# Performance work log

Measured on AMD Instinct MI355X. Metric: run time of the kernel, lower is better.

Reference implementation:

```python
import jax, jax.numpy as jnp
import numpy as np
from jax import lax

EPOCHS = 3
D_IN, D_OUT = 20, 18
_BN_EPS = 1e-5
_RECT_EPS = 1e-4


def _sym(a):
    return 0.5 * (a + jnp.swapaxes(a, -1, -2))


def _logm(a):
    s, u = jnp.linalg.eigh(_sym(a))
    return jnp.einsum('...ij,...j,...kj->...ik', u, jnp.log(s), u)


def _expm(a):
    s, u = jnp.linalg.eigh(_sym(a))
    return jnp.einsum('...ij,...j,...kj->...ik', u, jnp.exp(s), u)


def _rectify(a):
    # SPDRectified: clamp eigenvalues at epsilon
    s, u = jnp.linalg.eigh(_sym(a))
    s = jnp.maximum(s, _RECT_EPS)
    return jnp.einsum('...ij,...j,...kj->...ik', u, s, u)


def _bn(x, g, b):
    # training-mode BatchNorm2d (biased variance, as torch uses for normalization)
    m = x.mean(axis=(0, 2, 3), keepdims=True)
    v = x.var(axis=(0, 2, 3), keepdims=True)
    return (x - m) * lax.rsqrt(v + _BN_EPS) * g[None, :, None, None] + b[None, :, None, None]


def _patch_lens(n, epochs):
    base = n // epochs
    lens = [base] * epochs
    for i in range(n - base * epochs):
        lens[i] += 1
    return lens


def _forward(x, conv1_w, conv1_b, bn1_g, bn1_b, conv2_w, conv2_b, bn2_g, bn2_b,
             Wq, Wk, Wv, lin_w, lin_b):
    B = x.shape[0]
    # conv1: Conv2d(1, 22, (22, 1)) -- full contraction over the 22 EEG channels
    h = jnp.einsum('oh,bht->bot', conv1_w, x[:, 0]) + conv1_b[None, :, None]
    h = _bn(h[:, :, None, :], bn1_g, bn1_b)  # (B,22,1,T)
    # conv2: Conv2d(22, 20, (1, 12), padding=(0, 6)) -> time length T+1
    h = lax.conv_general_dilated(h, conv2_w, (1, 1), [(0, 0), (6, 6)],
                                 dimension_numbers=('NCHW', 'OIHW', 'NCHW'))
    h = h + conv2_b[None, :, None, None]
    h = _bn(h, bn2_g, bn2_b)
    sig = h[:, :, 0, :]  # (B, 20, T+1)
    # E2R: split time axis into EPOCHS patches, trace-normalized covariance per patch
    covs, off = [], 0
    eye = jnp.eye(D_IN, dtype=x.dtype)
    for L in _patch_lens(sig.shape[-1], EPOCHS):
        seg = sig[:, :, off:off + L]
        off += L
        seg = seg - seg.mean(axis=-1, keepdims=True)
        c = seg @ jnp.swapaxes(seg, -1, -2) / (L - 1)
        c = c / jnp.trace(c, axis1=-2, axis2=-1)[:, None, None]
        covs.append(c + 1e-5 * eye)
    cov = jnp.stack(covs, axis=1)  # (B, EPOCHS, 20, 20)
    # SPDTransform (bilinear congruence W^T X W) for Q, K, V
    Q = jnp.einsum('ia,bmij,jc->bmac', Wq, cov, Wq)
    K = jnp.einsum('ia,bmij,jc->bmac', Wk, cov, Wk)
    V = jnp.einsum('ia,bmij,jc->bmac', Wv, cov, Wv)
    logQ, logK, logV = _logm(Q), _logm(K), _logm(V)
    # log-Euclidean distance: sum of singular values of D D^T == ||D||_F^2
    # energy[b, i, j] = || logK[b,i] - logQ[b,j] ||_F^2 (matches the repeat/expand layout)
    diff = logK[:, :, None] - logQ[:, None, :]  # (B, m, m, d, d)
    energy = jnp.sum(diff * diff, axis=(-1, -2))  # (B, m, m)
    f = 1.0 / (1.0 + jnp.log1p(energy))
    prob = jax.nn.softmax(f, axis=-2)      # softmax over dim=-2 (the K index)
    prob = jnp.swapaxes(prob, -1, -2)      # permute(0, 2, 1)
    # LogEuclideanMean: weighted mean in log domain, then matrix exp
    mean_log = jnp.einsum('bpi,bikl->bpkl', prob, logV)
    out = _expm(mean_log)
    out = _rectify(out)
    tang = _logm(out)
    ri, ci = np.triu_indices(D_OUT)
    feat = tang[:, :, ri, ci].reshape(B, -1)  # (B, EPOCHS * 171)
    return feat @ lin_w.T + lin_b


def setup_inputs():
    key = jax.random.key(0)
    ks = jax.random.split(key, 16)
    B, C, T = 1024, 22, 438
    f32 = jnp.float32
    return {
        'x': jax.random.normal(ks[0], (B, 1, C, T), f32),
        'conv1_w': 0.1 * jax.random.normal(ks[1], (22, 22), f32),
        'conv1_b': 0.1 * jax.random.normal(ks[2], (22,), f32),
        'bn1_g': 1.0 + 0.1 * jax.random.normal(ks[3], (22,), f32),
        'bn1_b': 0.1 * jax.random.normal(ks[4], (22,), f32),
        'conv2_w': 0.05 * jax.random.normal(ks[5], (20, 22, 1, 12), f32),
        'conv2_b': 0.1 * jax.random.normal(ks[6], (20,), f32),
        'bn2_g': 1.0 + 0.1 * jax.random.normal(ks[7], (20,), f32),
        'bn2_b': 0.1 * jax.random.normal(ks[8], (20,), f32),
        'Wq': jnp.linalg.qr(jax.random.normal(ks[9], (20, 18), f32))[0],
        'Wk': jnp.linalg.qr(jax.random.normal(ks[10], (20, 18), f32))[0],
        'Wv': jnp.linalg.qr(jax.random.normal(ks[11], (20, 18), f32))[0],
        'lin_w': 0.05 * jax.random.normal(ks[12], (4, 9 * 19 * EPOCHS), f32),
        'lin_b': jnp.zeros((4,), f32),
    }


def reference(x, conv1_w, conv1_b, bn1_g, bn1_b, conv2_w, conv2_b, bn2_g, bn2_b,
              Wq, Wk, Wv, lin_w, lin_b):
    return _forward(x, conv1_w, conv1_b, bn1_g, bn1_b, conv2_w, conv2_b,
                    bn2_g, bn2_b, Wq, Wk, Wv, lin_w, lin_b)
```

## Files before the change

kernel.cpp:

```cpp
#include <hip/hip_runtime.h>
#include <cmath>

#define B_ 1024
#define CIN_ 22
#define T1_ 438
#define COUT_ 20
#define T2_ 439

#define OFF_S 0
#define OFF_M 32
#define OFF_SUM2 576
#define OFF_SSQ2 608
#define OFF_A2 640
#define OFF_ACC_END 704
#define OFF_C 1024
#define OFF_WEFF (OFF_C + B_*3*400)
#define OFF_BPRE (OFF_WEFF + 5280)

__global__ __launch_bounds__(256) void k_zero(float* ws){
  for(int i=threadIdx.x; i<OFF_ACC_END; i+=256) ws[i]=0.f;
}

__global__ __launch_bounds__(256) void k_moment(const float* __restrict__ x, float* __restrict__ ws){
  __shared__ float xs[CIN_][440];
  int b=blockIdx.x;
  const float* xb = x + (size_t)b*CIN_*T1_;
  for(int i=threadIdx.x;i<CIN_*T1_;i+=256){
    int h=i/T1_, t=i-h*T1_;
    xs[h][t]=xb[i];
  }
  if(threadIdx.x<CIN_){ xs[threadIdx.x][438]=0.f; xs[threadIdx.x][439]=0.f; }
  __syncthreads();
  for(int tgt=threadIdx.x; tgt<275; tgt+=256){
    if(tgt<253){
      int r=tgt, i=0;
      while(true){ int c=CIN_-i; if(r<c) break; r-=c; i++; }
      int j=i+r;
      const float4* ri=(const float4*)&xs[i][0];
      const float4* rj=(const float4*)&xs[j][0];
      float acc=0.f;
      for(int t=0;t<110;t++){
        float4 a=ri[t], bb=rj[t];
        acc += a.x*bb.x + a.y*bb.y + a.z*bb.z + a.w*bb.w;
      }
      atomicAdd(&ws[OFF_M + i*CIN_ + j], acc);
    } else {
      int c=tgt-253;
      const float4* rc=(const float4*)&xs[c][0];
      float acc=0.f;
      for(int t=0;t<110;t++){
        float4 a=rc[t];
        acc += a.x + a.y + a.z + a.w;
      }
      atomicAdd(&ws[OFF_S + c], acc);
    }
  }
}

__global__ __launch_bounds__(256) void k_prep(const float* __restrict__ w1, const float* __restrict__ cb1,
                                              const float* __restrict__ g1, const float* __restrict__ bb1,
                                              const float* __restrict__ w2, float* __restrict__ ws){
  __shared__ float a1s[CIN_], e1s[CIN_];
  int tid=threadIdx.x;
  if(tid<CIN_){
    int c=tid;
    const double N = (double)B_*T1_;
    double wS=0.0, wMw=0.0;
    for(int h=0;h<CIN_;h++) wS += (double)w1[c*CIN_+h]*(double)ws[OFF_S+h];
    for(int h=0;h<CIN_;h++){
      for(int h2=0;h2<CIN_;h2++){
        int i=h<h2?h:h2, j=h<h2?h2:h;
        wMw += (double)w1[c*CIN_+h]*(double)w1[c*CIN_+h2]*(double)ws[OFF_M+i*CIN_+j];
      }
    }
    double bc=cb1[c];
    double mean=wS/N+bc;
    double ex2=(wMw+2.0*bc*wS)/N+bc*bc;
    double var=ex2-mean*mean;
    double a1=(double)g1[c]/sqrt(var+1e-5);
    double d1=(double)bb1[c]-mean*a1;
    a1s[c]=(float)a1;
    e1s[c]=(float)(a1*bc+d1);
  }
  __syncthreads();
  for(int idx=tid; idx<5280; idx+=256){
    int o=idx/264, r=idx-o*264, h=r/12, k=r-h*12;
    float s=0.f;
    for(int i=0;i<CIN_;i++) s += w2[(o*CIN_+i)*12+k]*a1s[i]*w1[i*CIN_+h];
    ws[OFF_WEFF+idx]=s;
  }
  if(tid<COUT_){
    float pre=0.f;
    ws[OFF_BPRE+tid*13+0]=0.f;
    for(int k=0;k<12;k++){
      float wb=0.f;
      for(int i=0;i<CIN_;i++) wb += w2[(tid*CIN_+i)*12+k]*e1s[i];
      pre += wb;
      ws[OFF_BPRE+tid*13+k+1]=pre;
    }
  }
}

__global__ __launch_bounds__(256) void k_cov(const float* __restrict__ x,
                                             float* __restrict__ ws){
  __shared__ float Wl[5280];
  __shared__ float preL[COUT_][13];
  __shared__ float xs[CIN_][168];
  __shared__ float h2w[COUT_][156];
  __shared__ float pmu[COUT_];
  int b=blockIdx.x, tid=threadIdx.x;
  for(int i=tid;i<5280;i+=256) Wl[i]=ws[OFF_WEFF+i];
  for(int i=tid;i<260;i+=256) ((float*)preL)[i]=ws[OFF_BPRE+i];
  int pi=0,pj=0;
  if(tid<210){ int r=tid,i=0; while(true){int c=COUT_-i; if(r<c)break; r-=c; i++;} pi=i; pj=i+r; }
  int sc = tid-210;
  float ac1=0.f, ac2=0.f;
  const float* xb = x + (size_t)b*CIN_*T1_;
  int o = tid/12, cch = tid-12*o;
  int t0 = cch*13;
  for(int p=0;p<3;p++){
    const int off = (p==0)?0:((p==1)?147:293);
    const int L = (p==0)?147:146;
    __syncthreads();
    for(int idx=tid; idx<CIN_*168; idx+=256){
      int h=idx/168, c2=idx-h*168;
      int gxt = off-6+c2;
      xs[h][c2] = (c2<167 && gxt>=0 && gxt<T1_) ? xb[h*T1_+gxt] : 0.f;
    }
    __syncthreads();
    if(tid<240){
      float acc[13];
      #pragma unroll
      for(int j=0;j<13;j++){
        int gt = off+t0+j;
        int kmin = 6-gt; kmin = kmin<0?0:kmin;
        int kmax = 443-gt; kmax = kmax>11?11:kmax;
        acc[j] = (kmax>=kmin)? preL[o][kmax+1]-preL[o][kmin] : 0.f;
      }
      const float* Wo = &Wl[o*264];
      for(int h=0;h<CIN_;h++){
        float xw[24];
        #pragma unroll
        for(int c2=0;c2<24;c2++) xw[c2]=xs[h][t0+c2];
        const float* Wh = Wo + h*12;
        #pragma unroll
        for(int k=0;k<12;k++){
          float w=Wh[k];
          #pragma unroll
          for(int j=0;j<13;j++) acc[j] += w*xw[j+k];
        }
      }
      #pragma unroll
      for(int j=0;j<13;j++) if(t0+j<L) h2w[o][t0+j]=acc[j];
    } else {
      int npad = 156-L;
      for(int z=tid-240; z<COUT_*npad; z+=16){
        int oo=z/npad, c2=z-oo*npad;
        h2w[oo][L+c2]=0.f;
      }
    }
    __syncthreads();
    float s=0.f;
    if(tid<210){
      const float4* ri=(const float4*)&h2w[pi][0];
      const float4* rj=(const float4*)&h2w[pj][0];
      for(int t=0;t<39;t++){
        float4 a=ri[t], bb=rj[t];
        s += a.x*bb.x + a.y*bb.y + a.z*bb.z + a.w*bb.w;
      }
    } else if(sc>=0 && sc<COUT_){
      const float4* rc=(const float4*)&h2w[sc][0];
      float s1=0.f,s2=0.f;
      for(int t=0;t<39;t++){
        float4 a=rc[t];
        s1 += a.x+a.y+a.z+a.w;
        s2 += a.x*a.x+a.y*a.y+a.z*a.z+a.w*a.w;
      }
      ac1+=s1; ac2+=s2; pmu[sc]=s1/(float)L;
    }
    __syncthreads();
    if(tid<210){
      s -= (float)L*pmu[pi]*pmu[pj];
      float* Cb = ws + OFF_C + ((size_t)b*3+p)*400;
      Cb[pi*COUT_+pj]=s; Cb[pj*COUT_+pi]=s;
    }
  }
  if(sc>=0 && sc<COUT_){
    atomicAdd(&ws[OFF_SUM2+sc], ac1);
    atomicAdd(&ws[OFF_SSQ2+sc], ac2);
  }
}

__global__ void k_fin2(const float* __restrict__ g2, float* __restrict__ ws){
  int c=threadIdx.x; if(c>=COUT_) return;
  const double N=(double)B_*T2_;
  double m=ws[OFF_SUM2+c]/N;
  double v=ws[OFF_SSQ2+c]/N - m*m;
  ws[OFF_A2+c]=(float)((double)g2[c]/sqrt(v+1e-5));
}

__device__ __forceinline__ void bl_jacobi18(float own[18], float &dgo,
                                            int l18, int gb, bool act, int maxsweep){
  int self = gb + l18;
  for(int sweep=0; sweep<maxsweep; sweep++){
    { float d0=0.f,d1=0.f;
      #pragma unroll
      for(int k=0;k<18;k+=2){ d0+=own[k]*own[k]; d1+=own[k+1]*own[k+1]; }
      dgo=d0+d1;
    }
    float smax=0.f;
    for(int r=0;r<17;r++){
      int t = 2*r - l18;
      t += (t<0)?17:0;
      t -= (t>=17)?17:0;
      int pa = (l18==17)? r : ((t==l18)?17:t);
      int src = act ? (gb + pa) : self;
      float oth[18];
      #pragma unroll
      for(int k=0;k<18;k++) oth[k]=__shfl(own[k], src);
      float dgx = __shfl(dgo, src);
      float a0=0.f,a1=0.f;
      #pragma unroll
      for(int k=0;k<18;k+=2){ a0+=own[k]*oth[k]; a1+=own[k+1]*oth[k+1]; }
      float apq=a0+a1;
      bool isP = l18 < pa;
      float dgp = isP? dgo : dgx;
      float dgq = isP? dgx : dgo;
      float tau = __fdividef(dgq-dgp, 2.f*apq);
      float tt  = __fdividef(copysignf(1.f,tau), fabsf(tau)+sqrtf(1.f+tau*tau));
      float c   = rsqrtf(1.f+tt*tt);
      float s   = tt*c;
      bool  z   = (apq==0.f) || !act;
      tt=z?0.f:tt; c=z?1.f:c; s=z?0.f:s;
      smax=fmaxf(smax,fabsf(s));
      float sgn = isP ? -s : s;
      #pragma unroll
      for(int k=0;k<18;k++) own[k] = c*own[k] + sgn*oth[k];
      dgo = isP ? (dgp - tt*apq) : (dgq + tt*apq);
    }
    if(__all(smax<3e-3f)) break;
  }
  float d0=0.f,d1=0.f;
  #pragma unroll
  for(int k=0;k<18;k+=2){ d0+=own[k]*own[k]; d1+=own[k+1]*own[k+1]; }
  dgo=d0+d1;
}

#define F_A2S 0
#define F_WA 20
#define F_CS 1100
#define F_TT 2300
#define F_TRS 3434
#define F_LTR 3437
#define F_LG 3440
#define F_E9 6356
#define F_PROB 6365
#define F_SC 20
#define F_GL1 3098
#define F_ML 20
#define F_MC2 992
#define F_GL2 2018
#define F_FEAT 3440

__global__ __launch_bounds__(192) void k_fused(const float* __restrict__ Wq,
                                               const float* __restrict__ Wk,
                                               const float* __restrict__ Wv,
                                               const float* __restrict__ lw,
                                               const float* __restrict__ lb,
                                               float* __restrict__ ws,
                                               float* __restrict__ out){
  __shared__ float S[6374];
  int b=blockIdx.x, tid=threadIdx.x;
  int w=tid>>6, wl=tid&63;
  if(tid<20) S[F_A2S+tid]=ws[OFF_A2+tid];
  __syncthreads();
  for(int i=tid;i<1080;i+=192){
    int m=i/360, r=i-m*360, row=r/18;
    const float* W=(m==0)?Wq:((m==1)?Wk:Wv);
    S[F_WA+i]=W[r]*S[F_A2S+row];
  }
  {
    const float* Cb=ws+OFF_C+((size_t)b*3+w)*400;
    for(int i=wl;i<400;i+=64) S[F_CS+w*400+i]=Cb[i];
  }
  if(wl==0){
    float tr=0.f;
    #pragma unroll
    for(int i=0;i<20;i++) tr += S[F_CS+w*400+i*20+i]*S[F_A2S+i]*S[F_A2S+i];
    S[F_TRS+w]=tr;
    S[F_LTR+w]=logf(tr);
  }
  __syncthreads();
  for(int m=0;m<3;m++){
    const float* Wm=S+F_WA+m*360;
    const float* Cw=S+F_CS+w*400;
    float* Tw=S+F_TT+w*378;
    for(int idx=wl; idx<360; idx+=64){
      int a=idx/20, j=idx-a*20;
      float s=0.f;
      for(int i=0;i<20;i++) s += Wm[i*18+a]*Cw[i*20+j];
      Tw[a*21+j]=s;
    }
    __syncthreads();
    for(int idx=wl; idx<324; idx+=64){
      int a=idx/18, c=idx-a*18;
      float s=0.f;
      for(int j=0;j<20;j++) s += Tw[a*21+j]*Wm[j*18+c];
      S[F_LG + m*972 + w*324 + idx]=s;
    }
    __syncthreads();
  }
  int g=wl/18, l18=wl-18*g;
  bool act=(g<3);
  float tr_w=S[F_TRS+w], ltr_w=S[F_LTR+w];
  float sh=1e-5f*tr_w;
  float own[18], dgo=0.f;
  if(act){
    const float* Ag=S+F_LG+g*972+w*324;
    #pragma unroll
    for(int k=0;k<18;k++)
      own[k]=0.5f*(Ag[k*18+l18]+Ag[l18*18+k]) + ((k==l18)?sh:0.f);
  } else {
    #pragma unroll
    for(int k=0;k<18;k++) own[k]=0.f;
  }
  __syncthreads();
  bl_jacobi18(own,dgo,l18,g*18,act,8);
  float dp=fmaxf(dgo,1e-30f);
  float gv=__fdividef(0.5f*logf(dp)-ltr_w, dp);
  float* Mc1=S+F_SC+w*1026;
  float* gl1=S+F_GL1+w*54;
  if(act){
    #pragma unroll
    for(int k=0;k<18;k++) Mc1[g*342 + k*19 + l18]=own[k];
    gl1[g*18+l18]=gv;
  }
  if(wl<54){
    int mat=g, i=l18;
    float w18[18];
    #pragma unroll
    for(int k=0;k<18;k++) w18[k]=gl1[mat*18+k]*Mc1[mat*342+i*19+k];
    float* ob=S+F_LG+mat*972+w*324+i*18;
    for(int j=0;j<18;j++){
      float s=0.f;
      #pragma unroll
      for(int k=0;k<18;k++) s += w18[k]*Mc1[mat*342+j*19+k];
      ob[j]=s;
    }
  }
  __syncthreads();
  if(tid<36){
    int d=tid>>2, sub=tid&3;
    int ii=d/3, p=d-ii*3;
    const float* kk=S+F_LG+972+ii*324+sub*81;
    const float* qq=S+F_LG+p*324+sub*81;
    float s=0.f;
    for(int el=0;el<81;el++){ float dd=kk[el]-qq[el]; s+=dd*dd; }
    s += __shfl_xor(s,1); s += __shfl_xor(s,2);
    if(sub==0) S[F_E9+d]=s;
  }
  __syncthreads();
  if(tid<3){
    int p=tid;
    float f0=1.f/(1.f+log1pf(S[F_E9+0+p]));
    float f1=1.f/(1.f+log1pf(S[F_E9+3+p]));
    float f2=1.f/(1.f+log1pf(S[F_E9+6+p]));
    float mx=fmaxf(f0,fmaxf(f1,f2));
    float x0=expf(f0-mx), x1=expf(f1-mx), x2=expf(f2-mx);
    float inv=1.f/(x0+x1+x2);
    S[F_PROB+p*3+0]=x0*inv; S[F_PROB+p*3+1]=x1*inv; S[F_PROB+p*3+2]=x2*inv;
  }
  __syncthreads();
  for(int idx=tid; idx<972; idx+=192){
    int p=idx/324, el=idx-p*324;
    const float* LV=S+F_LG+1944;
    S[F_ML+idx]=S[F_PROB+p*3+0]*LV[el]+S[F_PROB+p*3+1]*LV[324+el]+S[F_PROB+p*3+2]*LV[648+el];
  }
  __syncthreads();
  bool act2=(wl<18);
  float own2[18], dgo2=0.f;
  if(act2){
    const float* Ag=S+F_ML+w*324;
    #pragma unroll
    for(int k=0;k<18;k++)
      own2[k]=0.5f*(Ag[k*18+wl]+Ag[wl*18+k]) + ((k==wl)?12.f:0.f);
  } else {
    #pragma unroll
    for(int k=0;k<18;k++) own2[k]=0.f;
  }
  bl_jacobi18(own2,dgo2,wl,0,act2,8);
  float lam=sqrtf(fmaxf(dgo2,1e-12f));
  float gv2=__fdividef(fmaxf(lam-12.f,-9.2103404f), fmaxf(dgo2,1e-12f));
  if(act2){
    #pragma unroll
    for(int k=0;k<18;k++) S[F_MC2 + w*342 + k*19 + wl]=own2[k];
    S[F_GL2 + w*18 + wl]=gv2;
  }
  __syncthreads();
  if(tid<54){
    int mat=tid/18, i=tid-mat*18;
    float w18[18];
    #pragma unroll
    for(int k=0;k<18;k++) w18[k]=S[F_GL2+mat*18+k]*S[F_MC2+mat*342+i*19+k];
    int base = mat*171 + (i*18 - (i*(i-1))/2) - i;
    for(int j=i;j<18;j++){
      float s=0.f;
      #pragma unroll
      for(int k=0;k<18;k++) s += w18[k]*S[F_MC2+mat*342+j*19+k];
      S[F_FEAT+base+j]=s;
    }
  }
  __syncthreads();
  if(tid<64){
    int j4 = tid&3, chunk = tid>>2;
    float s=0.f;
    const float* wj = lw + j4*513;
    for(int k=chunk; k<513; k+=16) s += S[F_FEAT+k]*wj[k];
    s += __shfl_xor(s,4); s += __shfl_xor(s,8);
    s += __shfl_xor(s,16); s += __shfl_xor(s,32);
    if(chunk==0) out[b*4+j4] = s + lb[j4];
  }
}

extern "C" void kernel_launch(void* const* d_in, const int* in_sizes, int n_in,
                              void* d_out, int out_size, void* d_ws, size_t ws_size,
                              hipStream_t stream){
  const float* x  =(const float*)d_in[0];
  const float* w1 =(const float*)d_in[1];
  const float* cb1=(const float*)d_in[2];
  const float* g1 =(const float*)d_in[3];
  const float* bb1=(const float*)d_in[4];
  const float* w2 =(const float*)d_in[5];
  const float* g2 =(const float*)d_in[7];
  const float* Wq =(const float*)d_in[9];
  const float* Wk =(const float*)d_in[10];
  const float* Wv =(const float*)d_in[11];
  const float* lw =(const float*)d_in[12];
  const float* lb =(const float*)d_in[13];
  float* ws=(float*)d_ws;
  float* out=(float*)d_out;

  k_zero<<<1,256,0,stream>>>(ws);
  k_moment<<<B_,256,0,stream>>>(x,ws);
  k_prep<<<1,256,0,stream>>>(w1,cb1,g1,bb1,w2,ws);
  k_cov<<<B_,256,0,stream>>>(x,ws);
  k_fin2<<<1,64,0,stream>>>(g2,ws);
  k_fused<<<B_,192,0,stream>>>(Wq,Wk,Wv,lw,lb,ws,out);
}
```

Baseline: 429.1 us.

## Register-tile channel moment accumulation per wave and pack final Jacobi into one wave

The moment kernel no longer stages each batch's 22x438 input in shared memory with one thread per channel pair. Each of four waves now owns a fixed subset of the 275 pair/sum outputs, streams time samples straight into registers using a constexpr pair table, and reduces with wave shuffles before issuing atomics. The final 18x18 Jacobi step now packs its three matrices into a single wave as lane groups of 18 instead of spreading them across three waves. The moment change is meant to cut shared-memory traffic and serial per-thread dot products, at the cost of heavy register use (up to 69 accumulators plus 22 inputs) and limited occupancy from launch_bounds(256,1).

After: 780.4 us. 81.8% more time.

```diff
diff --git a/kernel.cpp b/kernel.cpp
--- a/kernel.cpp
+++ b/kernel.cpp
@@ -21,39 +21,78 @@
   for(int i=threadIdx.x; i<OFF_ACC_END; i+=256) ws[i]=0.f;
 }
 
-__global__ __launch_bounds__(256) void k_moment(const float* __restrict__ x, float* __restrict__ ws){
-  __shared__ float xs[CIN_][440];
-  int b=blockIdx.x;
-  const float* xb = x + (size_t)b*CIN_*T1_;
-  for(int i=threadIdx.x;i<CIN_*T1_;i+=256){
-    int h=i/T1_, t=i-h*T1_;
-    xs[h][t]=xb[i];
-  }
-  if(threadIdx.x<CIN_){ xs[threadIdx.x][438]=0.f; xs[threadIdx.x][439]=0.f; }
-  __syncthreads();
-  for(int tgt=threadIdx.x; tgt<275; tgt+=256){
-    if(tgt<253){
-      int r=tgt, i=0;
-      while(true){ int c=CIN_-i; if(r<c) break; r-=c; i++; }
-      int j=i+r;
-      const float4* ri=(const float4*)&xs[i][0];
-      const float4* rj=(const float4*)&xs[j][0];
-      float acc=0.f;
-      for(int t=0;t<110;t++){
-        float4 a=ri[t], bb=rj[t];
-        acc += a.x*bb.x + a.y*bb.y + a.z*bb.z + a.w*bb.w;
-      }
-      atomicAdd(&ws[OFF_M + i*CIN_ + j], acc);
-    } else {
-      int c=tgt-253;
-      const float4* rc=(const float4*)&xs[c][0];
-      float acc=0.f;
-      for(int t=0;t<110;t++){
-        float4 a=rc[t];
-        acc += a.x + a.y + a.z + a.w;
-      }
-      atomicAdd(&ws[OFF_S + c], acc);
-    }
+struct PTab { short pi[276]; short pj[276]; };
+constexpr PTab mkptab(){
+  PTab t{};
+  int n=0;
+  for(int i=0;i<22;i++) for(int j=i;j<22;j++){ t.pi[n]=(short)i; t.pj[n]=(short)j; n++; }
+  for(int c=0;c<22;c++){ t.pi[n]=(short)c; t.pj[n]=-1; n++; }
+  t.pi[275]=0; t.pj[275]=0;
+  return t;
+}
+constexpr PTab PT = mkptab();
+
+template<int W>
+__device__ __forceinline__ void mom_wave(const float* __restrict__ xb,
+                                         float* __restrict__ ws, int lane){
+  constexpr int base = W*69;
+  constexpr int cnt = (275-base < 69) ? (275-base) : 69;
+  float acc[cnt];
+  #pragma unroll
+  for(int p=0;p<cnt;p++) acc[p]=0.f;
+  float xc[22];
+  for(int c=0;c<6;c++){
+    int t=c*64+lane;
+    #pragma unroll
+    for(int h=0;h<22;h++) xc[h]=xb[h*T1_+t];
+    #pragma unroll
+    for(int p=0;p<cnt;p++){
+      float xi = xc[PT.pi[base+p]];
+      float xj = (PT.pj[base+p]<0) ? 1.f : xc[PT.pj[base+p]];
+      acc[p] += xi*xj;
+    }
+  }
+  {
+    int t=384+lane;
+    bool v = t<T1_;
+    int tc = v ? t : (T1_-1);
+    float msk = v ? 1.f : 0.f;
+    #pragma unroll
+    for(int h=0;h<22;h++) xc[h]=xb[h*T1_+tc]*msk;
+    #pragma unroll
+    for(int p=0;p<cnt;p++){
+      float xi = xc[PT.pi[base+p]];
+      float xj = (PT.pj[base+p]<0) ? 1.f : xc[PT.pj[base+p]];
+      acc[p] += xi*xj;
+    }
+  }
+  #pragma unroll
+  for(int p=0;p<cnt;p++){
+    float v=acc[p];
+    v+=__shfl_xor(v,1); v+=__shfl_xor(v,2); v+=__shfl_xor(v,4);
+    v+=__shfl_xor(v,8); v+=__shfl_xor(v,16); v+=__shfl_xor(v,32);
+    acc[p]=v;
+  }
+  if(lane==0){
+    #pragma unroll
+    for(int p=0;p<cnt;p++){
+      constexpr_if_helper:;
+      int i=PT.pi[base+p], j=PT.pj[base+p];
+      if(j<0) atomicAdd(&ws[OFF_S+i], acc[p]);
+      else    atomicAdd(&ws[OFF_M+i*CIN_+j], acc[p]);
+    }
+  }
+}
+
+__global__ __launch_bounds__(256,1) void k_moment(const float* __restrict__ x,
+                                                  float* __restrict__ ws){
+  int w=threadIdx.x>>6, lane=threadIdx.x&63;
+  const float* xb = x + (size_t)blockIdx.x*CIN_*T1_;
+  switch(w){
+    case 0: mom_wave<0>(xb,ws,lane); break;
+    case 1: mom_wave<1>(xb,ws,lane); break;
+    case 2: mom_wave<2>(xb,ws,lane); break;
+    default: mom_wave<3>(xb,ws,lane); break;
   }
 }
 
@@ -377,24 +416,27 @@
     S[F_ML+idx]=S[F_PROB+p*3+0]*LV[el]+S[F_PROB+p*3+1]*LV[324+el]+S[F_PROB+p*3+2]*LV[648+el];
   }
   __syncthreads();
-  bool act2=(wl<18);
-  float own2[18], dgo2=0.f;
-  if(act2){
-    const float* Ag=S+F_ML+w*324;
-    #pragma unroll
-    for(int k=0;k<18;k++)
-      own2[k]=0.5f*(Ag[k*18+wl]+Ag[wl*18+k]) + ((k==wl)?12.f:0.f);
-  } else {
-    #pragma unroll
-    for(int k=0;k<18;k++) own2[k]=0.f;
-  }
-  bl_jacobi18(own2,dgo2,wl,0,act2,8);
-  float lam=sqrtf(fmaxf(dgo2,1e-12f));
-  float gv2=__fdividef(fmaxf(lam-12.f,-9.2103404f), fmaxf(dgo2,1e-12f));
-  if(act2){
-    #pragma unroll
-    for(int k=0;k<18;k++) S[F_MC2 + w*342 + k*19 + wl]=own2[k];
-    S[F_GL2 + w*18 + wl]=gv2;
+  if(w==0){
+    int g2=wl/18, l2=wl-18*g2;
+    bool act2=(g2<3);
+    float own2[18], dgo2=0.f;
+    if(act2){
+      const float* Ag=S+F_ML+g2*324;
+      #pragma unroll
+      for(int k=0;k<18;k++)
+        own2[k]=0.5f*(Ag[k*18+l2]+Ag[l2*18+k]) + ((k==l2)?12.f:0.f);
+    } else {
+      #pragma unroll
+      for(int k=0;k<18;k++) own2[k]=0.f;
+    }
+    bl_jacobi18(own2,dgo2,l2,g2*18,act2,8);
+    float lam=sqrtf(fmaxf(dgo2,1e-12f));
+    float gv2=__fdividef(fmaxf(lam-12.f,-9.2103404f), fmaxf(dgo2,1e-12f));
+    if(act2){
+      #pragma unroll
+      for(int k=0;k<18;k++) S[F_MC2 + g2*342 + k*19 + l2]=own2[k];
+      S[F_GL2 + g2*18 + l2]=gv2;
+    }
   }
   __syncthreads();
   if(tid<54){
```

## Split covariance kernel per patch, read weights from global, pack Jacobi into one wave

Applied to the files above, without the earlier changes.

k_cov now launches one block per (batch, patch) instead of looping over the three patches inside a block. This triples the block count and drops the per-block staging of the 5280-float effective weight into shared memory; weights are read directly from global/L2 instead. The second eigen-solve in k_fused is packed so the three 18x18 matrices share one wave (wave 0) rather than one wave each. k_moment pads the shared rows to 444 and loops over 111 float4s. The trade-off is that x gets reloaded and the atomics fire per patch, and the global weight reads may be slower than LDS reads.

Result: faster. 398.9 us (-7.1%).

```diff
diff --git a/kernel.cpp b/kernel.cpp
--- a/kernel.cpp
+++ b/kernel.cpp
@@ -22,16 +22,19 @@
 }
 
 __global__ __launch_bounds__(256) void k_moment(const float* __restrict__ x, float* __restrict__ ws){
-  __shared__ float xs[CIN_][440];
-  int b=blockIdx.x;
+  __shared__ float xs[CIN_][444];
+  int b=blockIdx.x, tid=threadIdx.x;
   const float* xb = x + (size_t)b*CIN_*T1_;
-  for(int i=threadIdx.x;i<CIN_*T1_;i+=256){
+  for(int i=tid;i<CIN_*T1_;i+=256){
     int h=i/T1_, t=i-h*T1_;
     xs[h][t]=xb[i];
   }
-  if(threadIdx.x<CIN_){ xs[threadIdx.x][438]=0.f; xs[threadIdx.x][439]=0.f; }
-  __syncthreads();
-  for(int tgt=threadIdx.x; tgt<275; tgt+=256){
+  if(tid<CIN_){
+    #pragma unroll
+    for(int t=T1_;t<444;t++) xs[tid][t]=0.f;
+  }
+  __syncthreads();
+  for(int tgt=tid; tgt<275; tgt+=256){
     if(tgt<253){
       int r=tgt, i=0;
       while(true){ int c=CIN_-i; if(r<c) break; r-=c; i++; }
@@ -39,7 +42,7 @@
       const float4* ri=(const float4*)&xs[i][0];
       const float4* rj=(const float4*)&xs[j][0];
       float acc=0.f;
-      for(int t=0;t<110;t++){
+      for(int t=0;t<111;t++){
         float4 a=ri[t], bb=rj[t];
         acc += a.x*bb.x + a.y*bb.y + a.z*bb.z + a.w*bb.w;
       }
@@ -48,7 +51,7 @@
       int c=tgt-253;
       const float4* rc=(const float4*)&xs[c][0];
       float acc=0.f;
-      for(int t=0;t<110;t++){
+      for(int t=0;t<111;t++){
         float4 a=rc[t];
         acc += a.x + a.y + a.z + a.w;
       }
@@ -103,91 +106,84 @@
 
 __global__ __launch_bounds__(256) void k_cov(const float* __restrict__ x,
                                              float* __restrict__ ws){
-  __shared__ float Wl[5280];
-  __shared__ float preL[COUT_][13];
+  __shared__ float preL[260];
   __shared__ float xs[CIN_][168];
   __shared__ float h2w[COUT_][156];
   __shared__ float pmu[COUT_];
-  int b=blockIdx.x, tid=threadIdx.x;
-  for(int i=tid;i<5280;i+=256) Wl[i]=ws[OFF_WEFF+i];
-  for(int i=tid;i<260;i+=256) ((float*)preL)[i]=ws[OFF_BPRE+i];
+  int blk=blockIdx.x, tid=threadIdx.x;
+  int b=blk/3, p=blk-3*b;
+  const int off = (p==0)?0:((p==1)?147:293);
+  const int L = (p==0)?147:146;
+  for(int i=tid;i<260;i+=256) preL[i]=ws[OFF_BPRE+i];
+  const float* xb = x + (size_t)b*CIN_*T1_;
+  for(int idx=tid; idx<CIN_*168; idx+=256){
+    int h=idx/168, c2=idx-h*168;
+    int gxt = off-6+c2;
+    xs[h][c2] = (c2<167 && gxt>=0 && gxt<T1_) ? xb[h*T1_+gxt] : 0.f;
+  }
+  __syncthreads();
+  int o = tid/12, cch = tid-12*o;
+  int t0 = cch*13;
+  if(tid<240){
+    float acc[13];
+    #pragma unroll
+    for(int j=0;j<13;j++){
+      int gt = off+t0+j;
+      int kmin = 6-gt; kmin = kmin<0?0:kmin;
+      int kmax = 443-gt; kmax = kmax>11?11:kmax;
+      acc[j] = (kmax>=kmin)? preL[o*13+kmax+1]-preL[o*13+kmin] : 0.f;
+    }
+    const float* Wo = ws + OFF_WEFF + o*264;
+    for(int h=0;h<CIN_;h++){
+      float xw[24];
+      #pragma unroll
+      for(int c2=0;c2<24;c2++) xw[c2]=xs[h][t0+c2];
+      const float* Wh = Wo + h*12;
+      #pragma unroll
+      for(int k=0;k<12;k++){
+        float w=Wh[k];
+        #pragma unroll
+        for(int j=0;j<13;j++) acc[j] += w*xw[j+k];
+      }
+    }
+    #pragma unroll
+    for(int j=0;j<13;j++) if(t0+j<L) h2w[o][t0+j]=acc[j];
+  } else {
+    int npad = 156-L;
+    for(int z=tid-240; z<COUT_*npad; z+=16){
+      int oo=z/npad, c2=z-oo*npad;
+      h2w[oo][L+c2]=0.f;
+    }
+  }
+  __syncthreads();
   int pi=0,pj=0;
   if(tid<210){ int r=tid,i=0; while(true){int c=COUT_-i; if(r<c)break; r-=c; i++;} pi=i; pj=i+r; }
   int sc = tid-210;
-  float ac1=0.f, ac2=0.f;
-  const float* xb = x + (size_t)b*CIN_*T1_;
-  int o = tid/12, cch = tid-12*o;
-  int t0 = cch*13;
-  for(int p=0;p<3;p++){
-    const int off = (p==0)?0:((p==1)?147:293);
-    const int L = (p==0)?147:146;
-    __syncthreads();
-    for(int idx=tid; idx<CIN_*168; idx+=256){
-      int h=idx/168, c2=idx-h*168;
-      int gxt = off-6+c2;
-      xs[h][c2] = (c2<167 && gxt>=0 && gxt<T1_) ? xb[h*T1_+gxt] : 0.f;
-    }
-    __syncthreads();
-    if(tid<240){
-      float acc[13];
-      #pragma unroll
-      for(int j=0;j<13;j++){
-        int gt = off+t0+j;
-        int kmin = 6-gt; kmin = kmin<0?0:kmin;
-        int kmax = 443-gt; kmax = kmax>11?11:kmax;
-        acc[j] = (kmax>=kmin)? preL[o][kmax+1]-preL[o][kmin] : 0.f;
-      }
-      const float* Wo = &Wl[o*264];
-      for(int h=0;h<CIN_;h++){
-        float xw[24];
-        #pragma unroll
-        for(int c2=0;c2<24;c2++) xw[c2]=xs[h][t0+c2];
-        const float* Wh = Wo + h*12;
-        #pragma unroll
-        for(int k=0;k<12;k++){
-          float w=Wh[k];
-          #pragma unroll
-          for(int j=0;j<13;j++) acc[j] += w*xw[j+k];
-        }
-      }
-      #pragma unroll
-      for(int j=0;j<13;j++) if(t0+j<L) h2w[o][t0+j]=acc[j];
-    } else {
-      int npad = 156-L;
-      for(int z=tid-240; z<COUT_*npad; z+=16){
-        int oo=z/npad, c2=z-oo*npad;
-        h2w[oo][L+c2]=0.f;
-      }
-    }
-    __syncthreads();
-    float s=0.f;
-    if(tid<210){
-      const float4* ri=(const float4*)&h2w[pi][0];
-      const float4* rj=(const float4*)&h2w[pj][0];
-      for(int t=0;t<39;t++){
-        float4 a=ri[t], bb=rj[t];
-        s += a.x*bb.x + a.y*bb.y + a.z*bb.z + a.w*bb.w;
-      }
-    } else if(sc>=0 && sc<COUT_){
-      const float4* rc=(const float4*)&h2w[sc][0];
-      float s1=0.f,s2=0.f;
-      for(int t=0;t<39;t++){
-        float4 a=rc[t];
-        s1 += a.x+a.y+a.z+a.w;
-        s2 += a.x*a.x+a.y*a.y+a.z*a.z+a.w*a.w;
-      }
-      ac1+=s1; ac2+=s2; pmu[sc]=s1/(float)L;
-    }
-    __syncthreads();
-    if(tid<210){
-      s -= (float)L*pmu[pi]*pmu[pj];
-      float* Cb = ws + OFF_C + ((size_t)b*3+p)*400;
-      Cb[pi*COUT_+pj]=s; Cb[pj*COUT_+pi]=s;
-    }
-  }
-  if(sc>=0 && sc<COUT_){
-    atomicAdd(&ws[OFF_SUM2+sc], ac1);
-    atomicAdd(&ws[OFF_SSQ2+sc], ac2);
+  float s=0.f;
+  if(tid<210){
+    const float4* ri=(const float4*)&h2w[pi][0];
+    const float4* rj=(const float4*)&h2w[pj][0];
+    for(int t=0;t<39;t++){
+      float4 a=ri[t], bb=rj[t];
+      s += a.x*bb.x + a.y*bb.y + a.z*bb.z + a.w*bb.w;
+    }
+  } else if(sc>=0 && sc<COUT_){
+    const float4* rc=(const float4*)&h2w[sc][0];
+    float s1=0.f,s2=0.f;
+    for(int t=0;t<39;t++){
+      float4 a=rc[t];
+      s1 += a.x+a.y+a.z+a.w;
+      s2 += a.x*a.x+a.y*a.y+a.z*a.z+a.w*a.w;
+    }
+    pmu[sc]=s1/(float)L;
+    atomicAdd(&ws[OFF_SUM2+sc], s1);
+    atomicAdd(&ws[OFF_SSQ2+sc], s2);
+  }
+  __syncthreads();
+  if(tid<210){
+    s -= (float)L*pmu[pi]*pmu[pj];
+    float* Cb = ws + OFF_C + (size_t)blk*400;
+    Cb[pi*COUT_+pj]=s; Cb[pj*COUT_+pi]=s;
   }
 }
 
@@ -377,24 +373,27 @@
     S[F_ML+idx]=S[F_PROB+p*3+0]*LV[el]+S[F_PROB+p*3+1]*LV[324+el]+S[F_PROB+p*3+2]*LV[648+el];
   }
   __syncthreads();
-  bool act2=(wl<18);
-  float own2[18], dgo2=0.f;
-  if(act2){
-    const float* Ag=S+F_ML+w*324;
-    #pragma unroll
-    for(int k=0;k<18;k++)
-      own2[k]=0.5f*(Ag[k*18+wl]+Ag[wl*18+k]) + ((k==wl)?12.f:0.f);
-  } else {
-    #pragma unroll
-    for(int k=0;k<18;k++) own2[k]=0.f;
-  }
-  bl_jacobi18(own2,dgo2,wl,0,act2,8);
-  float lam=sqrtf(fmaxf(dgo2,1e-12f));
-  float gv2=__fdividef(fmaxf(lam-12.f,-9.2103404f), fmaxf(dgo2,1e-12f));
-  if(act2){
-    #pragma unroll
-    for(int k=0;k<18;k++) S[F_MC2 + w*342 + k*19 + wl]=own2[k];
-    S[F_GL2 + w*18 + wl]=gv2;
+  if(w==0){
+    int g2=wl/18, l2=wl-18*g2;
+    bool act2=(g2<3);
+    float own2[18], dgo2=0.f;
+    if(act2){
+      const float* Ag=S+F_ML+g2*324;
+      #pragma unroll
+      for(int k=0;k<18;k++)
+        own2[k]=0.5f*(Ag[k*18+l2]+Ag[l2*18+k]) + ((k==l2)?12.f:0.f);
+    } else {
+      #pragma unroll
+      for(int k=0;k<18;k++) own2[k]=0.f;
+    }
+    bl_jacobi18(own2,dgo2,l2,g2*18,act2,8);
+    float lam=sqrtf(fmaxf(dgo2,1e-12f));
+    float gv2=__fdividef(fmaxf(lam-12.f,-9.2103404f), fmaxf(dgo2,1e-12f));
+    if(act2){
+      #pragma unroll
+      for(int k=0;k<18;k++) S[F_MC2 + g2*342 + k*19 + l2]=own2[k];
+      S[F_GL2 + g2*18 + l2]=gv2;
+    }
   }
   __syncthreads();
   if(tid<54){
@@ -443,7 +442,7 @@
   k_zero<<<1,256,0,stream>>>(ws);
   k_moment<<<B_,256,0,stream>>>(x,ws);
   k_prep<<<1,256,0,stream>>>(w1,cb1,g1,bb1,w2,ws);
-  k_cov<<<B_,256,0,stream>>>(x,ws);
+  k_cov<<<3072,256,0,stream>>>(x,ws);
   k_fin2<<<1,64,0,stream>>>(g2,ws);
   k_fused<<<B_,192,0,stream>>>(Wq,Wk,Wv,lw,lb,ws,out);
 }
```
